# Performance work log

Hardware: AMD Instinct MI355X
Metric: run time of the kernel (lower is better)

The kernel has to match this reference:

```python
import jax, jax.numpy as jnp
import numpy as np

H = 16
D_MODEL = 1024
D_K = D_MODEL // H
NEG = -1e9


def setup_inputs() -> dict:
    key = jax.random.key(0)
    ks = jax.random.split(key, 12)
    B, S, D = 2, 2048, D_MODEL
    scale = 1.0 / np.sqrt(D)
    inp = {
        "query": jax.random.normal(ks[0], (B, S, D), jnp.float32),
        "key": jax.random.normal(ks[1], (B, S, D), jnp.float32),
        "value": jax.random.normal(ks[2], (B, S, D), jnp.float32),
        "mask": jax.random.randint(ks[3], (B, S, S), 0, 2, jnp.int32),
        # four Linear(d_model, d_model) layers: q, k, v, out projections
        "Wq": jax.random.normal(ks[4], (D, D), jnp.float32) * scale,
        "bq": jnp.zeros((D,), jnp.float32),
        "Wk": jax.random.normal(ks[5], (D, D), jnp.float32) * scale,
        "bk": jnp.zeros((D,), jnp.float32),
        "Wv": jax.random.normal(ks[6], (D, D), jnp.float32) * scale,
        "bv": jnp.zeros((D,), jnp.float32),
        "Wo": jax.random.normal(ks[7], (D, D), jnp.float32) * scale,
        "bo": jnp.zeros((D,), jnp.float32),
    }
    return inp


def reference(query, key, value, mask, Wq, bq, Wk, bk, Wv, bv, Wo, bo):
    B, S, D = query.shape
    # QKV projections, then split into heads: [B, H, S, D_K]
    def proj(x, W, b):
        return (x @ W + b).reshape(B, S, H, D_K).transpose(0, 2, 1, 3)

    q = proj(query, Wq, bq)
    k = proj(key, Wk, bk)
    v = proj(value, Wv, bv)

    # scaled dot-product attention; scale by sqrt(d_k) (query.size(-1) after split)
    scores = jnp.einsum("bhqd,bhkd->bhqk", q, k) / np.sqrt(D_K)
    scores = jnp.where(mask[:, None, :, :] == 0, NEG, scores)
    p = jax.nn.softmax(scores, axis=-1)  # dropout is identity in eval mode
    x = jnp.einsum("bhqk,bhkd->bhqd", p, v)

    # merge heads and apply output projection
    x = x.transpose(0, 2, 1, 3).reshape(B, S, H * D_K)
    return x @ Wo + bo
```

## Files before the change

### kernel.cpp

```cpp
#include <hip/hip_runtime.h>

typedef _Float16 f16;
typedef __attribute__((ext_vector_type(2))) _Float16 f16x2;
typedef __attribute__((ext_vector_type(4))) _Float16 f16x4;
typedef __attribute__((ext_vector_type(8))) _Float16 f16x8;
typedef __attribute__((ext_vector_type(4))) float f32x4;
typedef __attribute__((ext_vector_type(2))) __fp16 fp16x2;

#define MFMA16(A_, B_, C_) __builtin_amdgcn_mfma_f32_16x16x32_f16(A_, B_, C_, 0, 0, 0)
#define EXP2(x) __builtin_amdgcn_exp2f(x)

#define NHEAD 16
#define SEQ 2048
#define DM 1024
#define DK 64
#define NBATCH 2
#define M_TOT (NBATCH * SEQ)
#define CSC 0.18033688011112042f

#define GLDS(gp, lp)                                                                     \
    __builtin_amdgcn_global_load_lds((const __attribute__((address_space(1))) void*)(gp), \
                                     (__attribute__((address_space(3))) void*)(lp), 16, 0, 0)

__global__ __launch_bounds__(256) void prep_k(
    const int* __restrict__ mask, unsigned long long* __restrict__ mp,
    const float* __restrict__ Wq, const float* __restrict__ Wk,
    const float* __restrict__ Wv, const float* __restrict__ Wo, f16* __restrict__ Wt) {
    __shared__ float T[64][65];
    const int z = blockIdx.z, bx = blockIdx.x, tid = threadIdx.x;
    if (z == 0) {
        const int zz = bx >> 8, t = bx & 255;
        const float* W = zz == 0 ? Wq : (zz == 1 ? Wk : (zz == 2 ? Wv : Wo));
        const float wsc = zz == 0 ? CSC : 1.0f;
        f16* out = Wt + (size_t)zz * DM * DM;
        const int k0 = (t >> 4) * 64, n0 = (t & 15) * 64;
        const int r = tid >> 2, q = tid & 3;
        const float4* s = (const float4*)&W[(size_t)(k0 + r) * DM + n0 + q * 16];
        float4 v0 = s[0], v1 = s[1], v2 = s[2], v3 = s[3];
        T[r][q * 16 + 0] = v0.x; T[r][q * 16 + 1] = v0.y; T[r][q * 16 + 2] = v0.z; T[r][q * 16 + 3] = v0.w;
        T[r][q * 16 + 4] = v1.x; T[r][q * 16 + 5] = v1.y; T[r][q * 16 + 6] = v1.z; T[r][q * 16 + 7] = v1.w;
        T[r][q * 16 + 8] = v2.x; T[r][q * 16 + 9] = v2.y; T[r][q * 16 + 10] = v2.z; T[r][q * 16 + 11] = v2.w;
        T[r][q * 16 + 12] = v3.x; T[r][q * 16 + 13] = v3.y; T[r][q * 16 + 14] = v3.z; T[r][q * 16 + 15] = v3.w;
        __syncthreads();
        f16x8 h0, h1;
#pragma unroll
        for (int j = 0; j < 8; ++j) {
            h0[j] = (f16)(T[q * 16 + j][r] * wsc);
            h1[j] = (f16)(T[q * 16 + 8 + j][r] * wsc);
        }
        *(f16x8*)&out[(size_t)(n0 + r) * DM + k0 + q * 16] = h0;
        *(f16x8*)&out[(size_t)(n0 + r) * DM + k0 + q * 16 + 8] = h1;
    } else {
        if (bx >= 512) return;
        int lane = tid & 63;
        int gw = (bx * 256 + tid) >> 6;
        const int nw = (512 * 256) >> 6;
        const int nwords = NBATCH * SEQ * (SEQ / 64);
        for (int w = gw; w < nwords; w += nw) {
            int v = mask[(size_t)w * 64 + lane];
            unsigned long long bits = __ballot(v != 0);
            if (lane == 0) mp[w] = bits;
        }
    }
}

__device__ __forceinline__ void gemm_core(const f16* __restrict__ A, const f16* __restrict__ Bt,
                                          int m0, int n0, f16* Al, f16* Bl, f32x4 acc[4][4], int tid) {
    const int lane = tid & 63;
    const int wv = tid >> 6;
    const int wr = wv >> 1, wc = wv & 1;
    const int g = lane >> 4, c = lane & 15;

    for (int k0 = 0; k0 < DM; k0 += 64) {
#pragma unroll
        for (int j = 0; j < 4; ++j) {
            int chunk = j * 256 + tid;
            int row = chunk >> 3, cc = chunk & 7;
            int ccs = cc ^ (row & 7);
            GLDS(&A[(size_t)(m0 + row) * DM + k0 + ccs * 8], &Al[chunk * 8]);
        }
#pragma unroll
        for (int j = 0; j < 4; ++j) {
            int chunk = j * 256 + tid;
            int row = chunk >> 3, cc = chunk & 7;
            int ccs = cc ^ (row & 7);
            GLDS(&Bt[(size_t)(n0 + row) * DM + k0 + ccs * 8], &Bl[chunk * 8]);
        }
        __syncthreads();
#pragma unroll
        for (int ks = 0; ks < 2; ++ks) {
            f16x8 af[4], bf[4];
#pragma unroll
            for (int mi = 0; mi < 4; ++mi) {
                int row = wr * 64 + mi * 16 + c;
                af[mi] = *(const f16x8*)&Al[row * 64 + ((ks * 4 + g) ^ (row & 7)) * 8];
            }
#pragma unroll
            for (int ni = 0; ni < 4; ++ni) {
                int row = wc * 64 + ni * 16 + c;
                bf[ni] = *(const f16x8*)&Bl[row * 64 + ((ks * 4 + g) ^ (row & 7)) * 8];
            }
#pragma unroll
            for (int mi = 0; mi < 4; ++mi)
#pragma unroll
                for (int ni = 0; ni < 4; ++ni)
                    acc[mi][ni] = MFMA16(af[mi], bf[ni], acc[mi][ni]);
        }
        __syncthreads();
    }
}

__device__ __forceinline__ void xcd_swizzle(int& bx, int& by, int gdx) {
    int lin = by * gdx + bx;
    int nl = (lin & 7) * 32 + (lin >> 3);
    bx = nl % gdx;
    by = nl / gdx;
}

__global__ __launch_bounds__(256) void gemm_qkv2_k(
    const float* __restrict__ Xq, const float* __restrict__ Xk, const float* __restrict__ Xv,
    const f16* __restrict__ Wt, const float* __restrict__ bq, const float* __restrict__ bk,
    const float* __restrict__ bv, f16* __restrict__ Qh, f16* __restrict__ Kh, f16* __restrict__ VhT) {
    __shared__ float Al[128 * 16 * 4];
    __shared__ f16 Bl[128 * 64];
    const int which = blockIdx.z;
    const float* A = which == 0 ? Xq : (which == 1 ? Xk : Xv);
    const f16* Bt = Wt + (size_t)which * DM * DM;
    const float* bias = which == 0 ? bq : (which == 1 ? bk : bv);

    const int tid = threadIdx.x, lane = tid & 63, wv = tid >> 6;
    const int wr = wv >> 1, wc = wv & 1, g = lane >> 4, c = lane & 15;
    int bx = blockIdx.x, by = blockIdx.y;
    xcd_swizzle(bx, by, gridDim.x);
    const int m0 = by * 128, n0 = bx * 128;

    f32x4 acc[4][4] = {};

    for (int k0 = 0; k0 < DM; k0 += 64) {
#pragma unroll
        for (int j = 0; j < 8; ++j) {
            int q = j * 256 + tid;
            int row = q >> 4, cc = q & 15;
            int ccs = cc ^ (row & 15);
            GLDS(&A[(size_t)(m0 + row) * DM + k0 + ccs * 4], &Al[q * 4]);
        }
#pragma unroll
        for (int j = 0; j < 4; ++j) {
            int chunk = j * 256 + tid;
            int row = chunk >> 3, cc = chunk & 7;
            int ccs = cc ^ (row & 7);
            GLDS(&Bt[(size_t)(n0 + row) * DM + k0 + ccs * 8], &Bl[chunk * 8]);
        }
        __syncthreads();
#pragma unroll
        for (int ks = 0; ks < 2; ++ks) {
            f16x8 af[4], bf[4];
#pragma unroll
            for (int mi = 0; mi < 4; ++mi) {
                int row = wr * 64 + mi * 16 + c;
                int cb = ks * 8 + g * 2;
                f32x4 a0 = *(const f32x4*)&Al[(row * 16 + (cb ^ (row & 15))) * 4];
                f32x4 a1 = *(const f32x4*)&Al[(row * 16 + ((cb + 1) ^ (row & 15))) * 4];
                f16x8 h;
#pragma unroll
                for (int t2 = 0; t2 < 4; ++t2) {
                    h[t2] = (f16)a0[t2];
                    h[4 + t2] = (f16)a1[t2];
                }
                af[mi] = h;
            }
#pragma unroll
            for (int ni = 0; ni < 4; ++ni) {
                int row = wc * 64 + ni * 16 + c;
                bf[ni] = *(const f16x8*)&Bl[row * 64 + ((ks * 4 + g) ^ (row & 7)) * 8];
            }
#pragma unroll
            for (int mi = 0; mi < 4; ++mi)
#pragma unroll
                for (int ni = 0; ni < 4; ++ni)
                    acc[mi][ni] = MFMA16(af[mi], bf[ni], acc[mi][ni]);
        }
        __syncthreads();
    }

    const float bsc = which == 0 ? CSC : 1.0f;
    if (which == 2) {
#pragma unroll
        for (int ni = 0; ni < 4; ++ni) {
            int n = n0 + wc * 64 + ni * 16 + c;
            float bias_n = bias[n];
            int hh = n >> 6, d = n & 63;
#pragma unroll
            for (int mi = 0; mi < 4; ++mi) {
                int mbase = m0 + wr * 64 + mi * 16 + g * 4;
                int bb = mbase >> 11, s = mbase & (SEQ - 1);
                f16x4 o;
#pragma unroll
                for (int r = 0; r < 4; ++r) o[r] = (f16)(acc[mi][ni][r] + bias_n);
                *(f16x4*)&VhT[(((size_t)(bb * NHEAD + hh)) * DK + d) * SEQ + s] = o;
            }
        }
    } else {
        f16* OUT = which == 0 ? Qh : Kh;
#pragma unroll
        for (int ni = 0; ni < 4; ++ni) {
            int n = n0 + wc * 64 + ni * 16 + c;
            float bias_n = bias[n] * bsc;
            int hh = n >> 6, d = n & 63;
#pragma unroll
            for (int mi = 0; mi < 4; ++mi) {
                int mbase = m0 + wr * 64 + mi * 16 + g * 4;
#pragma unroll
                for (int r = 0; r < 4; ++r) {
                    int m = mbase + r;
                    int bb = m >> 11, s = m & (SEQ - 1);
                    OUT[(((size_t)(bb * NHEAD + hh)) * SEQ + s) * DK + d] = (f16)(acc[mi][ni][r] + bias_n);
                }
            }
        }
    }
}

__global__ __launch_bounds__(256) void gemm_out2_k(
    const f16* __restrict__ Xo, const f16* __restrict__ Wto, const float* __restrict__ bo,
    float* __restrict__ OUT) {
    __shared__ f16 Al[128 * 64];
    __shared__ f16 Bl[128 * 64];
    const int tid = threadIdx.x, lane = tid & 63, wv = tid >> 6;
    const int wr = wv >> 1, wc = wv & 1, g = lane >> 4, c = lane & 15;
    int bx = blockIdx.x, by = blockIdx.y;
    xcd_swizzle(bx, by, gridDim.x);
    const int m0 = by * 128, n0 = bx * 128;

    f32x4 acc[4][4] = {};
    gemm_core(Xo, Wto, m0, n0, Al, Bl, acc, tid);

#pragma unroll
    for (int ni = 0; ni < 4; ++ni) {
        int n = n0 + wc * 64 + ni * 16 + c;
        float bias_n = bo[n];
#pragma unroll
        for (int mi = 0; mi < 4; ++mi) {
            int mbase = m0 + wr * 64 + mi * 16 + g * 4;
#pragma unroll
            for (int r = 0; r < 4; ++r) {
                int m = mbase + r;
                OUT[(size_t)m * DM + n] = acc[mi][ni][r] + bias_n;
            }
        }
    }
}

#define QBLK 128
#define KVB 128
#define NIT (SEQ / KVB)

__global__ __launch_bounds__(512) void attn_k(
    const f16* __restrict__ Qh, const f16* __restrict__ Kh, const f16* __restrict__ VhT,
    const unsigned long long* __restrict__ mp, f16* __restrict__ Xo) {
    __shared__ f16 Kl[2][2][4096];
    __shared__ f16 Vl[2][2][4096];

    const int tid = threadIdx.x, lane = tid & 63, wv = tid >> 6;
    const int g = lane >> 4, c = lane & 15;
    const int lin = blockIdx.x;
    const int key = lin & 31;
    const int qt = lin >> 5;
    const int hh = key & (NHEAD - 1), b = key >> 4;
    const size_t headoff = ((size_t)(b * NHEAD + hh)) * SEQ * DK;
    const f16* Qb = Qh + headoff;
    const f16* Kb = Kh + headoff;
    const f16* VbT = VhT + headoff;

    const int srow = tid >> 3, scc = (tid & 7) ^ (srow & 7);
    const int kap = ((srow >> 4) & 1) * 32 + ((srow >> 2) & 3) * 8 + ((srow >> 5) & 1) * 4 + (srow & 3);

#define STAGE_ATTN(jj, pp)                                                                    \
    do {                                                                                      \
        GLDS(&Kb[(size_t)((jj)*KVB + kap) * DK + scc * 8], &Kl[pp][0][tid * 8]);              \
        GLDS(&Kb[(size_t)((jj)*KVB + 64 + kap) * DK + scc * 8], &Kl[pp][1][tid * 8]);         \
        GLDS(&VbT[(size_t)srow * SEQ + (jj)*KVB + scc * 8], &Vl[pp][0][tid * 8]);             \
        GLDS(&VbT[(size_t)srow * SEQ + (jj)*KVB + 64 + scc * 8], &Vl[pp][1][tid * 8]);        \
    } while (0)

    const int qrow = qt * QBLK + wv * 16 + c;
    f16x8 bq0 = *(const f16x8*)&Qb[(size_t)qrow * DK + g * 8];
    f16x8 bq1 = *(const f16x8*)&Qb[(size_t)qrow * DK + 32 + g * 8];

    f32x4 acc[4] = {};
    float l_run = 0.f;
    const fp16x2 ones = {(__fp16)1.0f, (__fp16)1.0f};

    const unsigned long long* mrow = mp + ((size_t)b * SEQ + qrow) * (SEQ / 64);
    unsigned long long wq_c0 = mrow[0], wq_c1 = mrow[1];

    STAGE_ATTN(0, 0);
    int p = 0;
    for (int j = 0; j < NIT; ++j) {
        __syncthreads();
        if (j + 1 < NIT) STAGE_ATTN(j + 1, p ^ 1);
        unsigned long long wq_n0 = (j + 1 < NIT) ? mrow[2 * j + 2] : 0ull;
        unsigned long long wq_n1 = (j + 1 < NIT) ? mrow[2 * j + 3] : 0ull;

#pragma unroll
        for (int u = 0; u < 2; ++u) {
            const f16* Klu = Kl[p][u];
            const f16* Vlu = Vl[p][u];
            unsigned long long wq_cur = u ? wq_c1 : wq_c0;

            f32x4 sc[4];
            __builtin_amdgcn_s_setprio(1);
#pragma unroll
            for (int nk = 0; nk < 4; ++nk) {
                int row = nk * 16 + c;
                f16x8 k0 = *(const f16x8*)&Klu[row * 64 + ((g ^ (row & 7)) * 8)];
                f16x8 k1 = *(const f16x8*)&Klu[row * 64 + (((4 + g) ^ (row & 7)) * 8)];
                f32x4 z = {};
                z = MFMA16(k0, bq0, z);
                z = MFMA16(k1, bq1, z);
                sc[nk] = z;
            }
            __builtin_amdgcn_s_setprio(0);

            unsigned long long wq_g = wq_cur >> (g * 8);
            union { unsigned int uu[4]; f16x8 v; } U0, U1;
#pragma unroll
            for (int nk = 0; nk < 4; ++nk) {
                unsigned int nib = (unsigned int)(wq_g >> ((nk & 1) * 32 + (nk >> 1) * 4)) & 0xFu;
                float p0 = EXP2(sc[nk][0]); p0 = (nib & 1u) ? p0 : 0.f;
                float p1 = EXP2(sc[nk][1]); p1 = (nib & 2u) ? p1 : 0.f;
                float p2 = EXP2(sc[nk][2]); p2 = (nib & 4u) ? p2 : 0.f;
                float p3 = EXP2(sc[nk][3]); p3 = (nib & 8u) ? p3 : 0.f;
                fp16x2 w01 = __builtin_amdgcn_cvt_pkrtz(p0, p1);
                fp16x2 w23 = __builtin_amdgcn_cvt_pkrtz(p2, p3);
                l_run = __builtin_amdgcn_fdot2(w01, ones, l_run, false);
                l_run = __builtin_amdgcn_fdot2(w23, ones, l_run, false);
                unsigned int uw01 = *(unsigned int*)&w01;
                unsigned int uw23 = *(unsigned int*)&w23;
                if (nk & 1) {
                    U1.uu[(nk >> 1) * 2] = uw01;
                    U1.uu[(nk >> 1) * 2 + 1] = uw23;
                } else {
                    U0.uu[(nk >> 1) * 2] = uw01;
                    U0.uu[(nk >> 1) * 2 + 1] = uw23;
                }
            }
            f16x8 pb0 = U0.v;
            f16x8 pb1 = U1.v;

            __builtin_amdgcn_s_setprio(1);
#pragma unroll
            for (int nd = 0; nd < 4; ++nd) {
                int row = nd * 16 + c;
                f16x8 v0 = *(const f16x8*)&Vlu[row * 64 + ((g ^ (row & 7)) * 8)];
                f16x8 v1 = *(const f16x8*)&Vlu[row * 64 + (((4 + g) ^ (row & 7)) * 8)];
                acc[nd] = MFMA16(v0, pb0, acc[nd]);
                acc[nd] = MFMA16(v1, pb1, acc[nd]);
            }
            __builtin_amdgcn_s_setprio(0);
        }

        wq_c0 = wq_n0;
        wq_c1 = wq_n1;
        p ^= 1;
    }

    l_run += __shfl_xor(l_run, 16);
    l_run += __shfl_xor(l_run, 32);

    {
        float inv = l_run > 0.f ? 1.0f / l_run : 0.f;
#pragma unroll
        for (int nd = 0; nd < 4; ++nd) {
            f16x4 o;
#pragma unroll
            for (int r = 0; r < 4; ++r) o[r] = (f16)(acc[nd][r] * inv);
            *(f16x4*)&Xo[((size_t)(b * SEQ) + qrow) * DM + hh * DK + nd * 16 + g * 4] = o;
        }
    }
#undef STAGE_ATTN
}

extern "C" void kernel_launch(void* const* d_in, const int* in_sizes, int n_in,
                              void* d_out, int out_size, void* d_ws, size_t ws_size,
                              hipStream_t stream) {
    const float* query = (const float*)d_in[0];
    const float* key_ = (const float*)d_in[1];
    const float* value = (const float*)d_in[2];
    const int* mask = (const int*)d_in[3];
    const float* Wq = (const float*)d_in[4];
    const float* bq = (const float*)d_in[5];
    const float* Wk = (const float*)d_in[6];
    const float* bk = (const float*)d_in[7];
    const float* Wv = (const float*)d_in[8];
    const float* bv = (const float*)d_in[9];
    const float* Wo = (const float*)d_in[10];
    const float* bo = (const float*)d_in[11];
    float* out = (float*)d_out;

    char* ws = (char*)d_ws;
    const size_t headsz = (size_t)NBATCH * NHEAD * SEQ * DK * sizeof(f16);
    unsigned long long* mp = (unsigned long long*)(ws);
    f16* Qh = (f16*)(ws + (1 << 20));
    f16* Kh = (f16*)(ws + (1 << 20) + headsz);
    f16* VhT = (f16*)(ws + (1 << 20) + 2 * headsz);
    f16* Xo = (f16*)(ws + (1 << 20) + 3 * headsz);
    f16* Wt = (f16*)(ws + (1 << 20) + 6 * headsz);

    hipLaunchKernelGGL(prep_k, dim3(1024, 1, 2), dim3(256), 0, stream,
                       mask, mp, Wq, Wk, Wv, Wo, Wt);
    hipLaunchKernelGGL(gemm_qkv2_k, dim3(DM / 128, M_TOT / 128, 3), dim3(256), 0, stream,
                       query, key_, value, Wt, bq, bk, bv, Qh, Kh, VhT);
    hipLaunchKernelGGL(attn_k, dim3(SEQ / QBLK * NHEAD * NBATCH), dim3(512), 0, stream,
                       Qh, Kh, VhT, mp, Xo);
    hipLaunchKernelGGL(gemm_out2_k, dim3(DM / 128, M_TOT / 128), dim3(256), 0, stream,
                       Xo, Wt + (size_t)3 * DM * DM, bo, out);
}
```

Baseline: 150.6 us.

## Double-buffer QKV GEMM LDS tiles with a halved K-step and a single barrier

The QKV projection GEMM now uses two LDS buffers, each with a K-tile of 32 instead of one buffer with a K-tile of 64. Global-to-LDS loads for the next K-step are issued right after the barrier, so they overlap the MFMA work on the current buffer. This also removes the second barrier per iteration. In exchange there are twice as many iterations and barriers per GEMM, and each barrier still waits for outstanding loads, which may limit how much overlap is achieved.

New measurement: 179.5 us. +19.2%, slower.

```diff
diff --git a/kernel.cpp b/kernel.cpp
--- a/kernel.cpp
+++ b/kernel.cpp
@@ -121,8 +121,8 @@
     const float* __restrict__ Xq, const float* __restrict__ Xk, const float* __restrict__ Xv,
     const f16* __restrict__ Wt, const float* __restrict__ bq, const float* __restrict__ bk,
     const float* __restrict__ bv, f16* __restrict__ Qh, f16* __restrict__ Kh, f16* __restrict__ VhT) {
-    __shared__ float Al[128 * 16 * 4];
-    __shared__ f16 Bl[128 * 64];
+    __shared__ float Al[2][128 * 8 * 4];
+    __shared__ f16 Bl[2][128 * 32];
     const int which = blockIdx.z;
     const float* A = which == 0 ? Xq : (which == 1 ? Xk : Xv);
     const f16* Bt = Wt + (size_t)which * DM * DM;
@@ -136,31 +136,35 @@
 
     f32x4 acc[4][4] = {};
 
-    for (int k0 = 0; k0 < DM; k0 += 64) {
-#pragma unroll
-        for (int j = 0; j < 8; ++j) {
-            int q = j * 256 + tid;
-            int row = q >> 4, cc = q & 15;
-            int ccs = cc ^ (row & 15);
-            GLDS(&A[(size_t)(m0 + row) * DM + k0 + ccs * 4], &Al[q * 4]);
-        }
-#pragma unroll
-        for (int j = 0; j < 4; ++j) {
-            int chunk = j * 256 + tid;
-            int row = chunk >> 3, cc = chunk & 7;
-            int ccs = cc ^ (row & 7);
-            GLDS(&Bt[(size_t)(n0 + row) * DM + k0 + ccs * 8], &Bl[chunk * 8]);
-        }
+#define STAGE_G(jj, pp)                                                                   \
+    do {                                                                                  \
+        int kk0 = (jj) * 32;                                                              \
+        _Pragma("unroll") for (int j = 0; j < 4; ++j) {                                   \
+            int q = j * 256 + tid;                                           \
+            int row = q >> 3, cc = q & 7;                                                 \
+            int ccs = cc ^ (row & 7);                                                     \
+            GLDS(&A[(size_t)(m0 + row) * DM + kk0 + ccs * 4], &Al[pp][q * 4]);            \
+        }                                                                                 \
+        _Pragma("unroll") for (int j = 0; j < 2; ++j) {                                   \
+            int q = j * 256 + tid;                                            \
+            int row = q >> 2, cc = q & 3;                                                 \
+            int ccs = cc ^ (row & 3);                                                     \
+            GLDS(&Bt[(size_t)(n0 + row) * DM + kk0 + ccs * 8], &Bl[pp][q * 8]);           \
+        }                                                                                 \
+    } while (0)
+
+    STAGE_G(0, 0);
+    int p = 0;
+    for (int j = 0; j < DM / 32; ++j) {
         __syncthreads();
-#pragma unroll
-        for (int ks = 0; ks < 2; ++ks) {
+        if (j + 1 < DM / 32) STAGE_G(j + 1, p ^ 1);
+        {
             f16x8 af[4], bf[4];
 #pragma unroll
             for (int mi = 0; mi < 4; ++mi) {
                 int row = wr * 64 + mi * 16 + c;
-                int cb = ks * 8 + g * 2;
-                f32x4 a0 = *(const f32x4*)&Al[(row * 16 + (cb ^ (row & 15))) * 4];
-                f32x4 a1 = *(const f32x4*)&Al[(row * 16 + ((cb + 1) ^ (row & 15))) * 4];
+                f32x4 a0 = *(const f32x4*)&Al[p][(row * 8 + ((g * 2) ^ (row & 7))) * 4];
+                f32x4 a1 = *(const f32x4*)&Al[p][(row * 8 + ((g * 2 + 1) ^ (row & 7))) * 4];
                 f16x8 h;
 #pragma unroll
                 for (int t2 = 0; t2 < 4; ++t2) {
@@ -172,7 +176,7 @@
 #pragma unroll
             for (int ni = 0; ni < 4; ++ni) {
                 int row = wc * 64 + ni * 16 + c;
-                bf[ni] = *(const f16x8*)&Bl[row * 64 + ((ks * 4 + g) ^ (row & 7)) * 8];
+                bf[ni] = *(const f16x8*)&Bl[p][row * 32 + (g ^ (row & 3)) * 8];
             }
 #pragma unroll
             for (int mi = 0; mi < 4; ++mi)
@@ -180,8 +184,9 @@
                 for (int ni = 0; ni < 4; ++ni)
                     acc[mi][ni] = MFMA16(af[mi], bf[ni], acc[mi][ni]);
         }
-        __syncthreads();
-    }
+        p ^= 1;
+    }
+#undef STAGE_G
 
     const float bsc = which == 0 ? CSC : 1.0f;
     if (which == 2) {
```
